# Optimization experiments

Measured on AMD Instinct MI355X. Metric: run time of the kernel, lower is better.

## Reference

```python
import jax, jax.numpy as jnp
import numpy as np

LAMBDA_SOFTMAX = 9.0
LAMBDA_LSE = 6.0
EPS = 1e-8
LEAKY_SLOPE = 0.1


def setup_inputs() -> dict:
    key = jax.random.key(0)
    k1, k2, k3, k4 = jax.random.split(key, 4)
    B, R, L, D = 256, 36, 40, 1024  # n_image=n_caption=B, n_regions, max_words, embed
    return {
        'pool_img': jax.random.normal(k1, (B, D), jnp.float32),
        'img_emb': jax.random.normal(k2, (B, R, D), jnp.float32),
        'pool_txt': jax.random.normal(k3, (B, D), jnp.float32),
        'cap_emb': jax.random.normal(k4, (B, L, D), jnp.float32),
    }


def _l2norm(x, axis):
    return x / (jnp.sqrt(jnp.sum(x * x, axis=axis, keepdims=True)) + EPS)


def _lse_reduce(m):
    # mul_(lambda_lse).exp_() ; sum over singleton dim ; log / lambda_lse
    return jnp.log(jnp.exp(m * LAMBDA_LSE)) / LAMBDA_LSE


def _text_score_one(cap_i, txt_poo_i, images):
    # cap_i: (L, d) query; images: (B, R, d) context. clipped_l2norm variant.
    attn = jnp.einsum('brd,ld->brl', images, cap_i)            # (B, R, L)
    attn = jax.nn.leaky_relu(attn, LEAKY_SLOPE)
    attn = _l2norm(attn, axis=2)                               # l2norm over queryL
    attn = jnp.swapaxes(attn, 1, 2)                            # (B, L, R)
    attn = jax.nn.softmax(attn * LAMBDA_SOFTMAX, axis=-1)      # softmax over regions
    wctx = jnp.einsum('blr,brd->bld', attn, images)            # (B, L, d)
    w12 = jnp.einsum('bld,d->bl', wctx, txt_poo_i)
    w1 = jnp.sqrt(jnp.sum(txt_poo_i * txt_poo_i))
    w2 = jnp.sqrt(jnp.sum(wctx * wctx, axis=2))
    sim = w12 / jnp.maximum(w1 * w2, EPS)                      # (B, L)
    return _lse_reduce(jnp.mean(sim, axis=1))                  # (B,)


def _image_score_one(cap_i, img_emb, img_poo):
    # query: img_emb (B, R, d); context: cap_i (L, d) broadcast over B.
    attn = jnp.einsum('ld,brd->blr', cap_i, img_emb)           # (B, L, R)
    attn = jax.nn.leaky_relu(attn, LEAKY_SLOPE)
    attn = _l2norm(attn, axis=2)                               # l2norm over regions
    attn = jnp.swapaxes(attn, 1, 2)                            # (B, R, L)
    attn = jax.nn.softmax(attn * LAMBDA_SOFTMAX, axis=-1)      # softmax over words
    wctx = jnp.einsum('brl,ld->brd', attn, cap_i)              # (B, R, d)
    w12 = jnp.einsum('brd,bd->br', wctx, img_poo)
    w1 = jnp.sqrt(jnp.sum(img_poo * img_poo, axis=1, keepdims=True))  # (B,1)
    w2 = jnp.sqrt(jnp.sum(wctx * wctx, axis=2))                # (B, R)
    sim = w12 / jnp.maximum(w1 * w2, EPS)
    return _lse_reduce(jnp.mean(sim, axis=1))                  # (B,)


def reference(pool_img, img_emb, pool_txt, cap_emb):
    # scores_t2i: loop over captions -> vmap; result (n_cap, n_image) -> transpose
    t2i = jax.vmap(_text_score_one, in_axes=(0, 0, None))(cap_emb, pool_txt, img_emb).T
    i2t = jax.vmap(_image_score_one, in_axes=(0, None, None))(cap_emb, img_emb, pool_img).T
    base = pool_img @ pool_txt.T
    return t2i + i2t + base
```

## Files before the change

kernel.cpp:

```cpp
#include <hip/hip_runtime.h>

typedef unsigned short u16;
typedef __attribute__((ext_vector_type(8))) short bf16x8;
typedef __attribute__((ext_vector_type(4))) float f32x4;

#define D_EMB 1024
#define NBAT  256
#define AS1 __attribute__((address_space(1)))
#define AS3 __attribute__((address_space(3)))

__device__ __forceinline__ u16 f2bf(float f){
    unsigned int u = __float_as_uint(f);
    unsigned int r = (u + 0x7fffu + ((u >> 16) & 1u)) >> 16;
    return (u16)r;
}
__device__ __forceinline__ float leaky(float x){ return x > 0.f ? x : 0.1f * x; }

__device__ __forceinline__ unsigned pack2(float a, float b){
    return (__float_as_uint(a) >> 16) | (__float_as_uint(b) & 0xffff0000u);
}

__global__ void pack_kernel(const float* __restrict__ pool_img, const float* __restrict__ img_emb,
                            const float* __restrict__ pool_txt, const float* __restrict__ cap_emb,
                            u16* __restrict__ imgw, u16* __restrict__ capw){
    int row = blockIdx.x;
    const float* src; u16* dst;
    if (row < NBAT * 37){
        int e = row / 37, rr = row - e * 37;
        src = (rr < 36) ? (img_emb + ((size_t)e * 36 + rr) * D_EMB) : (pool_img + (size_t)e * D_EMB);
        dst = imgw + (size_t)row * D_EMB;
    } else {
        int r2 = row - NBAT * 37;
        int e = r2 / 41, rr = r2 - e * 41;
        src = (rr < 40) ? (cap_emb + ((size_t)e * 40 + rr) * D_EMB) : (pool_txt + (size_t)e * D_EMB);
        dst = capw + (size_t)r2 * D_EMB;
    }
    int t = threadIdx.x;
    float4 v = ((const float4*)src)[t];
    unsigned long long pk = (unsigned long long)f2bf(v.x)
        | ((unsigned long long)f2bf(v.y) << 16)
        | ((unsigned long long)f2bf(v.z) << 32)
        | ((unsigned long long)f2bf(v.w) << 48);
    *(unsigned long long*)(dst + (size_t)t * 4) = pk;
}

__global__ void norm_kernel(const float* __restrict__ pool_img, const float* __restrict__ pool_txt,
                            float* __restrict__ w1i, float* __restrict__ w1t){
    __shared__ float red[256];
    int v = blockIdx.x;
    const float* src = (v < 256) ? (pool_img + (size_t)v * D_EMB)
                                 : (pool_txt + (size_t)(v - 256) * D_EMB);
    int t = threadIdx.x;
    float4 x = ((const float4*)src)[t];
    red[t] = x.x*x.x + x.y*x.y + x.z*x.z + x.w*x.w;
    __syncthreads();
    for (int off = 128; off > 0; off >>= 1){
        if (t < off) red[t] += red[t + off];
        __syncthreads();
    }
    if (t == 0){
        float n = sqrtf(red[0]);
        if (v < 256) w1i[v] = n; else w1t[v - 256] = n;
    }
}

__launch_bounds__(256, 2)
__global__ void gram_kernel(const u16* __restrict__ imgw, const u16* __restrict__ capw,
                            float* __restrict__ G, float* __restrict__ H){
    __shared__ __align__(16) char gsm[6144];
    int blk = blockIdx.x;
    int tid = threadIdx.x, lane = tid & 63;
    int wave = __builtin_amdgcn_readfirstlane(tid >> 6);
    int frow = lane & 15, q = lane >> 4;

    const u16* E; float* Gout; int R;
    if (blk < NBAT){ E = imgw + (size_t)blk * 37 * D_EMB; Gout = G + (size_t)blk * 1296; R = 36; }
    else { int b = blk - NBAT; E = capw + (size_t)b * 41 * D_EMB; Gout = H + (size_t)b * 1600; R = 40; }

    {
        uint4 z = {0u,0u,0u,0u};
        for (int off = tid * 16; off < 6144; off += 4096) *(uint4*)(gsm + off) = z;
    }

    const u16* gsrc[2]; int goff[2]; bool gval[2];
    #pragma unroll
    for (int j = 0; j < 2; ++j){
        int g = wave + j * 4;
        gval[j] = false; gsrc[j] = E; goff[j] = 0;
        if (g < 6){
            int kk = g / 3, t = g - kk * 3;
            int row = t * 16 + frow;
            gsrc[j] = E + (size_t)row * D_EMB + kk * 32 + q * 8;
            goff[j] = g * 1024;
            gval[j] = (row < R);
        }
    }

    int wm = wave >> 1, wn = wave & 1;
    int nTm = wm ? 1 : 2, nTn = wn ? 1 : 2;
    f32x4 acc[2][2];
    #pragma unroll
    for (int a = 0; a < 2; ++a)
        #pragma unroll
        for (int b = 0; b < 2; ++b) acc[a][b] = (f32x4){0.f,0.f,0.f,0.f};

    for (int c = 0; c < 16; ++c){
        __syncthreads();
        #pragma unroll
        for (int j = 0; j < 2; ++j){
            if (gval[j]){
                __builtin_amdgcn_global_load_lds(
                    (const AS1 void*)(const void*)(gsrc[j] + c * 64),
                    (AS3 void*)(void*)(gsm + goff[j] + lane * 16),
                    16, 0, 0);
            }
        }
        __syncthreads();
        #pragma unroll
        for (int kk = 0; kk < 2; ++kk){
            bf16x8 fA[2], fB[2];
            #pragma unroll
            for (int mi = 0; mi < 2; ++mi)
                if (mi < nTm) fA[mi] = *(const bf16x8*)(gsm + ((kk * 3 + (wm + mi * 2)) * 64 + lane) * 16);
            #pragma unroll
            for (int ni = 0; ni < 2; ++ni)
                if (ni < nTn) fB[ni] = *(const bf16x8*)(gsm + ((kk * 3 + (wn + ni * 2)) * 64 + lane) * 16);
            #pragma unroll
            for (int mi = 0; mi < 2; ++mi)
                if (mi < nTm)
                    #pragma unroll
                    for (int ni = 0; ni < 2; ++ni)
                        if (ni < nTn)
                            acc[mi][ni] = __builtin_amdgcn_mfma_f32_16x16x32_bf16(
                                fA[mi], fB[ni], acc[mi][ni], 0, 0, 0);
        }
    }

    #pragma unroll
    for (int mi = 0; mi < 2; ++mi){
        if (mi < nTm){
            int tm = wm + mi * 2;
            #pragma unroll
            for (int ni = 0; ni < 2; ++ni){
                if (ni < nTn){
                    int tn = wn + ni * 2;
                    int col = tn * 16 + frow;
                    if (col < R){
                        #pragma unroll
                        for (int g = 0; g < 4; ++g){
                            int row = tm * 16 + q * 4 + g;
                            if (row < R) Gout[row * R + col] = acc[mi][ni][g];
                        }
                    }
                }
            }
        }
    }
}

template<int R>
__device__ __forceinline__ void chol_wave(const float* __restrict__ src,
                                          u16* __restrict__ dst, int lane){
    int r = lane;
    bool act = (r < R);
    const float* row = src + (size_t)(act ? r : 0) * R;
    float a[R];
    #pragma unroll
    for (int k = 0; k < R; ++k) a[k] = act ? row[k] : 0.f;
    #pragma unroll
    for (int j = 0; j < R; ++j){
        float ajj = __shfl(a[j], j);
        float inv = (ajj > 1e-12f) ? rsqrtf(ajj) : 0.f;
        float lrj = a[j] * inv;
        if (r < j || !act) lrj = 0.f;
        dst[j * 64 + lane] = f2bf(lrj);
        #pragma unroll
        for (int k = j + 1; k < R; ++k){
            float lkj = __shfl(lrj, k);
            a[k] = fmaf(-lrj, lkj, a[k]);
        }
    }
    #pragma unroll
    for (int j = R; j < 48; ++j) dst[j * 64 + lane] = 0;
}

__global__ void chol_kernel(const float* __restrict__ G, const float* __restrict__ H,
                            u16* __restrict__ Lbi, u16* __restrict__ Lbc){
    int lane = threadIdx.x & 63;
    int wave = threadIdx.x >> 6;
    int id = blockIdx.x * 4 + wave;
    if (id < NBAT) chol_wave<36>(G + (size_t)id * 1296, Lbi + (size_t)id * 3072, lane);
    else           chol_wave<40>(H + (size_t)(id - NBAT) * 1600, Lbc + (size_t)(id - NBAT) * 3072, lane);
}

__launch_bounds__(256, 5)
__global__ void fused_kernel(const u16* __restrict__ imgw, const u16* __restrict__ capw,
                             const u16* __restrict__ Lbi, const u16* __restrict__ Lbc,
                             const float* __restrict__ w1i, const float* __restrict__ w1t,
                             float* __restrict__ out){
    __shared__ __align__(16) char smem[26624];
    float* Call = (float*)smem;
    float* rnb  = (float*)(smem + 25160);
    float* cnb  = (float*)(smem + 25736);

    int tid  = threadIdx.x;
    int lane = tid & 63;
    int wave = __builtin_amdgcn_readfirstlane(tid >> 6);
    int frow = lane & 15, q = lane >> 4;

    int lin = blockIdx.x;
    int xcd = lin & 7;
    int s   = lin >> 3;
    int b_t = (xcd << 4) | (s & 15);
    int i_t = s >> 4;
    int b0 = b_t * 2, i0 = i_t * 2;
    const u16* Ag = imgw + (size_t)b0 * 37 * D_EMB;
    const u16* Bg = capw + (size_t)i0 * 41 * D_EMB;

    {
        uint4 z = {0u,0u,0u,0u};
        for (int off = tid * 16; off < 22528; off += 4096) *(uint4*)(smem + off) = z;
    }

    const u16* gsrc[3]; int goff[3]; bool gval[3];
    #pragma unroll
    for (int j = 0; j < 3; ++j){
        int g = wave + j * 4;
        gval[j] = false; gsrc[j] = Ag; goff[j] = 0;
        if (g < 11){
            if (g < 5){
                int row = g * 16 + frow;
                gsrc[j] = Ag + (size_t)row * D_EMB + q * 8;
                goff[j] = g * 1024;
                gval[j] = (row < 74);
            } else {
                int gb = g - 5;
                int row = gb * 16 + frow;
                gsrc[j] = Bg + (size_t)row * D_EMB + q * 8;
                goff[j] = 5120 + gb * 1024;
                gval[j] = (row < 82);
            }
        }
    }

    int wm = wave >> 1, wn = wave & 1;
    int nTm = wm ? 2 : 3;
    f32x4 acc[3][3];
    #pragma unroll
    for (int aa = 0; aa < 3; ++aa)
        #pragma unroll
        for (int bb = 0; bb < 3; ++bb) acc[aa][bb] = (f32x4){0.f, 0.f, 0.f, 0.f};

    __syncthreads();

    #pragma unroll
    for (int j = 0; j < 3; ++j){
        if (gval[j]){
            __builtin_amdgcn_global_load_lds(
                (const AS1 void*)(const void*)(gsrc[j]),
                (AS3 void*)(void*)(smem + goff[j] + lane * 16),
                16, 0, 0);
        }
    }
    __syncthreads();

    for (int c = 0; c < 32; ++c){
        if (c < 31){
            int nb = ((c + 1) & 1) * 11264;
            #pragma unroll
            for (int j = 0; j < 3; ++j){
                if (gval[j]){
                    __builtin_amdgcn_global_load_lds(
                        (const AS1 void*)(const void*)(gsrc[j] + (c + 1) * 32),
                        (AS3 void*)(void*)(smem + nb + goff[j] + lane * 16),
                        16, 0, 0);
                }
            }
        }
        int cb = (c & 1) * 11264;
        bf16x8 bfr[3];
        #pragma unroll
        for (int ni = 0; ni < 3; ++ni){
            int tn = wn + ni * 2;
            bfr[ni] = *(const bf16x8*)(smem + cb + 5120 + tn * 1024 + lane * 16);
        }
        #pragma unroll
        for (int mi = 0; mi < 3; ++mi){
            if (mi < nTm){
                int tm = wm + mi * 2;
                bf16x8 af = *(const bf16x8*)(smem + cb + tm * 1024 + lane * 16);
                #pragma unroll
                for (int ni = 0; ni < 3; ++ni){
                    acc[mi][ni] = __builtin_amdgcn_mfma_f32_16x16x32_bf16(
                        af, bfr[ni], acc[mi][ni], 0, 0, 0);
                }
            }
        }
        __syncthreads();
    }

    #pragma unroll
    for (int mi = 0; mi < 3; ++mi){
        if (mi < nTm){
            int tm = wm + mi * 2;
            #pragma unroll
            for (int ni = 0; ni < 3; ++ni){
                int tn = wn + ni * 2;
                int col = tn * 16 + frow;
                int rbase = tm * 16 + q * 4;
                if (col < 82){
                    #pragma unroll
                    for (int g = 0; g < 4; ++g){
                        int rowc = rbase + g;
                        if (rowc < 74) Call[rowc * 85 + col] = acc[mi][ni][g];
                    }
                }
            }
        }
    }
    __syncthreads();

    int pb = wave >> 1, pi = wave & 1;
    int bg = b0 + pb, ig = i0 + pi;
    const float* Sv = Call + (pb * 37) * 85 + pi * 41;
    const u16* Lb_t2i = Lbi + (size_t)bg * 3072;
    const u16* Lb_i2t = Lbc + (size_t)ig * 3072;

    {
        int r0 = (lane < 36) ? lane : 35;
        float s2 = 0.f;
        #pragma unroll
        for (int l = 0; l < 40; ++l){ float x = leaky(Sv[r0 * 85 + l]); s2 = fmaf(x, x, s2); }
        if (lane < 36) rnb[wave * 36 + lane] = 1.f / (sqrtf(s2) + 1e-8f);
    }
    {
        int l0 = (lane < 40) ? lane : 39;
        float s2 = 0.f;
        #pragma unroll
        for (int r = 0; r < 36; ++r){ float x = leaky(Sv[r * 85 + l0]); s2 = fmaf(x, x, s2); }
        if (lane < 40) cnb[wave * 40 + lane] = 1.f / (sqrtf(s2) + 1e-8f);
    }

    unsigned up[18]; float num1 = 0.f;
    {
        int lc = (lane < 40) ? lane : 39;
        #pragma unroll
        for (int r = 0; r < 36; r += 2){
            float x0 = leaky(Sv[r * 85 + lc]) * rnb[wave * 36 + r];
            float x1 = leaky(Sv[(r + 1) * 85 + lc]) * rnb[wave * 36 + r + 1];
            float e0 = __expf(9.0f * x0), e1 = __expf(9.0f * x1);
            num1 = fmaf(e0, Sv[r * 85 + 40], fmaf(e1, Sv[(r + 1) * 85 + 40], num1));
            up[r >> 1] = pack2(e0, e1);
        }
    }
    unsigned vp[20]; float num2 = 0.f;
    {
        int rc = (lane < 36) ? lane : 35;
        #pragma unroll
        for (int l = 0; l < 40; l += 2){
            float x0 = leaky(Sv[rc * 85 + l]) * cnb[wave * 40 + l];
            float x1 = leaky(Sv[rc * 85 + l + 1]) * cnb[wave * 40 + l + 1];
            float e0 = __expf(9.0f * x0), e1 = __expf(9.0f * x1);
            num2 = fmaf(e0, Sv[36 * 85 + l], fmaf(e1, Sv[36 * 85 + l + 1], num2));
            vp[l >> 1] = pack2(e0, e1);
        }
    }
    float base = Sv[36 * 85 + 40];
    __syncthreads();

    char* slice = smem + wave * 6144;
    int sxw = lane & 7;

    if (lane < 40){
        char* rp = slice + lane * 128;
        #pragma unroll
        for (int jj = 0; jj < 9; ++jj){
            int slot = jj >> 1, wi = (jj & 1) * 8;
            uint2 w; w.x = up[jj * 2]; w.y = up[jj * 2 + 1];
            *(uint2*)(rp + ((slot ^ sxw) * 16 + wi)) = w;
        }
        uint2 z2; z2.x = 0u; z2.y = 0u;
        *(uint2*)(rp + ((4 ^ sxw) * 16 + 8)) = z2;
        uint4 z4 = {0u,0u,0u,0u};
        #pragma unroll
        for (int slot = 5; slot < 8; ++slot)
            *(uint4*)(rp + ((slot ^ sxw) * 16)) = z4;
    }

    float tsum;
    {
        f32x4 pacc[3][3];
        #pragma unroll
        for (int aa = 0; aa < 3; ++aa)
            #pragma unroll
            for (int bb = 0; bb < 3; ++bb) pacc[aa][bb] = (f32x4){0.f,0.f,0.f,0.f};
        #pragma unroll
        for (int kk = 0; kk < 2; ++kk){
            bf16x8 afr[3];
            #pragma unroll
            for (int mt = 0; mt < 3; ++mt){
                int row = mt * 16 + frow;
                afr[mt] = *(const bf16x8*)(slice + row * 128 + (((kk * 4 + q) ^ (row & 7)) * 16));
            }
            #pragma unroll
            for (int nt = 0; nt < 3; ++nt){
                bf16x8 bfr = *(const bf16x8*)(Lb_t2i + (nt * 16 + frow) * 64 + kk * 32 + q * 8);
                #pragma unroll
                for (int mt = 0; mt < 3; ++mt)
                    pacc[mt][nt] = __builtin_amdgcn_mfma_f32_16x16x32_bf16(
                        afr[mt], bfr, pacc[mt][nt], 0, 0, 0);
            }
        }
        float w1 = w1t[ig];
        tsum = 0.f;
        #pragma unroll
        for (int mt = 0; mt < 3; ++mt){
            #pragma unroll
            for (int g = 0; g < 4; ++g){
                float sv = pacc[mt][0][g] * pacc[mt][0][g]
                         + pacc[mt][1][g] * pacc[mt][1][g];
                float t2 = pacc[mt][2][g] * pacc[mt][2][g];
                sv += (frow < 4) ? t2 : 0.f;
                sv += __shfl_xor(sv, 1); sv += __shfl_xor(sv, 2);
                sv += __shfl_xor(sv, 4); sv += __shfl_xor(sv, 8);
                int m = mt * 16 + 4 * q + g;
                float nm = __shfl(num1, m);
                float sim = nm / fmaxf(w1 * sqrtf(sv), 1e-8f);
                tsum += (m < 40) ? sim : 0.f;
            }
        }
        tsum += __shfl_xor(tsum, 16);
        tsum += __shfl_xor(tsum, 32);
    }

    if (lane < 36){
        char* rp = slice + lane * 128;
        #pragma unroll
        for (int jj = 0; jj < 10; ++jj){
            int slot = jj >> 1, wi = (jj & 1) * 8;
            uint2 w; w.x = vp[jj * 2]; w.y = vp[jj * 2 + 1];
            *(uint2*)(rp + ((slot ^ sxw) * 16 + wi)) = w;
        }
        uint4 z4 = {0u,0u,0u,0u};
        #pragma unroll
        for (int slot = 5; slot < 8; ++slot)
            *(uint4*)(rp + ((slot ^ sxw) * 16)) = z4;
    }

    float isum;
    {
        f32x4 pacc[3][3];
        #pragma unroll
        for (int aa = 0; aa < 3; ++aa)
            #pragma unroll
            for (int bb = 0; bb < 3; ++bb) pacc[aa][bb] = (f32x4){0.f,0.f,0.f,0.f};
        #pragma unroll
        for (int kk = 0; kk < 2; ++kk){
            bf16x8 afr[3];
            #pragma unroll
            for (int mt = 0; mt < 3; ++mt){
                int row = mt * 16 + frow;
                afr[mt] = *(const bf16x8*)(slice + row * 128 + (((kk * 4 + q) ^ (row & 7)) * 16));
            }
            #pragma unroll
            for (int nt = 0; nt < 3; ++nt){
                bf16x8 bfr = *(const bf16x8*)(Lb_i2t + (nt * 16 + frow) * 64 + kk * 32 + q * 8);
                #pragma unroll
                for (int mt = 0; mt < 3; ++mt)
                    pacc[mt][nt] = __builtin_amdgcn_mfma_f32_16x16x32_bf16(
                        afr[mt], bfr, pacc[mt][nt], 0, 0, 0);
            }
        }
        float w1 = w1i[bg];
        isum = 0.f;
        #pragma unroll
        for (int mt = 0; mt < 3; ++mt){
            #pragma unroll
            for (int g = 0; g < 4; ++g){
                float sv = pacc[mt][0][g] * pacc[mt][0][g]
                         + pacc[mt][1][g] * pacc[mt][1][g];
                float t2 = pacc[mt][2][g] * pacc[mt][2][g];
                sv += (frow < 8) ? t2 : 0.f;
                sv += __shfl_xor(sv, 1); sv += __shfl_xor(sv, 2);
                sv += __shfl_xor(sv, 4); sv += __shfl_xor(sv, 8);
                int m = mt * 16 + 4 * q + g;
                float nm = __shfl(num2, m);
                float sim = nm / fmaxf(w1 * sqrtf(sv), 1e-8f);
                isum += (m < 36) ? sim : 0.f;
            }
        }
        isum += __shfl_xor(isum, 16);
        isum += __shfl_xor(isum, 32);
    }

    if (lane == 0)
        out[bg * 256 + ig] = tsum * (1.f / 40.f) + isum * (1.f / 36.f) + base;
}

extern "C" void kernel_launch(void* const* d_in, const int* in_sizes, int n_in,
                              void* d_out, int out_size, void* d_ws, size_t ws_size,
                              hipStream_t stream){
    const float* pool_img = (const float*)d_in[0];
    const float* img_emb  = (const float*)d_in[1];
    const float* pool_txt = (const float*)d_in[2];
    const float* cap_emb  = (const float*)d_in[3];
    float* out = (float*)d_out;

    char* ws = (char*)d_ws;
    size_t o = 0;
    u16* imgw = (u16*)(ws + o);  o += (size_t)256 * 37 * 1024 * 2;
    u16* capw = (u16*)(ws + o);  o += (size_t)256 * 41 * 1024 * 2;
    float* G  = (float*)(ws + o); o += (size_t)256 * 36 * 36 * 4;
    float* H  = (float*)(ws + o); o += (size_t)256 * 40 * 40 * 4;
    float* w1i = (float*)(ws + o); o += 1024;
    float* w1t = (float*)(ws + o); o += 1024;
    u16* Lbi = (u16*)(ws + o); o += (size_t)256 * 48 * 64 * 2;
    u16* Lbc = (u16*)(ws + o); o += (size_t)256 * 48 * 64 * 2;

    pack_kernel<<<19968, 256, 0, stream>>>(pool_img, img_emb, pool_txt, cap_emb, imgw, capw);
    norm_kernel<<<512, 256, 0, stream>>>(pool_img, pool_txt, w1i, w1t);
    gram_kernel<<<512, 256, 0, stream>>>(imgw, capw, G, H);
    chol_kernel<<<128, 256, 0, stream>>>(G, H, Lbi, Lbc);
    fused_kernel<<<16384, 256, 0, stream>>>(imgw, capw, Lbi, Lbc, w1i, w1t, out);
}
```

Baseline: 872.6 us.

## Build MFMA A-fragments in registers and fold numerator into spare MFMA column

Exponentiated attention weights are now computed directly in the MFMA A-fragment layout in registers, replacing the earlier pass that wrote packed bf16 rows to a swizzled LDS slice and read them back. The per-row numerator (weights dotted with the pooled-vector projection) is no longer accumulated in fp32 on the side. It is obtained by placing the projection values in an unused B column of the last MFMA tile. This drops LDS stores and loads plus a barrier, but recomputes the exp and leaky_relu work for each fragment and computes the numerator in bf16 rather than fp32, which may change accuracy.

```diff
diff --git a/kernel.cpp b/kernel.cpp
--- a/kernel.cpp
+++ b/kernel.cpp
@@ -3,6 +3,7 @@
 typedef unsigned short u16;
 typedef __attribute__((ext_vector_type(8))) short bf16x8;
 typedef __attribute__((ext_vector_type(4))) float f32x4;
+typedef __attribute__((ext_vector_type(4))) unsigned u32x4;
 
 #define D_EMB 1024
 #define NBAT  256
@@ -340,52 +341,7 @@
         for (int r = 0; r < 36; ++r){ float x = leaky(Sv[r * 85 + l0]); s2 = fmaf(x, x, s2); }
         if (lane < 40) cnb[wave * 40 + lane] = 1.f / (sqrtf(s2) + 1e-8f);
     }
-
-    unsigned up[18]; float num1 = 0.f;
-    {
-        int lc = (lane < 40) ? lane : 39;
-        #pragma unroll
-        for (int r = 0; r < 36; r += 2){
-            float x0 = leaky(Sv[r * 85 + lc]) * rnb[wave * 36 + r];
-            float x1 = leaky(Sv[(r + 1) * 85 + lc]) * rnb[wave * 36 + r + 1];
-            float e0 = __expf(9.0f * x0), e1 = __expf(9.0f * x1);
-            num1 = fmaf(e0, Sv[r * 85 + 40], fmaf(e1, Sv[(r + 1) * 85 + 40], num1));
-            up[r >> 1] = pack2(e0, e1);
-        }
-    }
-    unsigned vp[20]; float num2 = 0.f;
-    {
-        int rc = (lane < 36) ? lane : 35;
-        #pragma unroll
-        for (int l = 0; l < 40; l += 2){
-            float x0 = leaky(Sv[rc * 85 + l]) * cnb[wave * 40 + l];
-            float x1 = leaky(Sv[rc * 85 + l + 1]) * cnb[wave * 40 + l + 1];
-            float e0 = __expf(9.0f * x0), e1 = __expf(9.0f * x1);
-            num2 = fmaf(e0, Sv[36 * 85 + l], fmaf(e1, Sv[36 * 85 + l + 1], num2));
-            vp[l >> 1] = pack2(e0, e1);
-        }
-    }
     float base = Sv[36 * 85 + 40];
-    __syncthreads();
-
-    char* slice = smem + wave * 6144;
-    int sxw = lane & 7;
-
-    if (lane < 40){
-        char* rp = slice + lane * 128;
-        #pragma unroll
-        for (int jj = 0; jj < 9; ++jj){
-            int slot = jj >> 1, wi = (jj & 1) * 8;
-            uint2 w; w.x = up[jj * 2]; w.y = up[jj * 2 + 1];
-            *(uint2*)(rp + ((slot ^ sxw) * 16 + wi)) = w;
-        }
-        uint2 z2; z2.x = 0u; z2.y = 0u;
-        *(uint2*)(rp + ((4 ^ sxw) * 16 + 8)) = z2;
-        uint4 z4 = {0u,0u,0u,0u};
-        #pragma unroll
-        for (int slot = 5; slot < 8; ++slot)
-            *(uint4*)(rp + ((slot ^ sxw) * 16)) = z4;
-    }
 
     float tsum;
     {
@@ -396,15 +352,43 @@
             for (int bb = 0; bb < 3; ++bb) pacc[aa][bb] = (f32x4){0.f,0.f,0.f,0.f};
         #pragma unroll
         for (int kk = 0; kk < 2; ++kk){
+            float rn[8];
+            #pragma unroll
+            for (int j = 0; j < 8; ++j){
+                int k = kk * 32 + q * 8 + j;
+                int kc = (k < 36) ? k : 35;
+                rn[j] = (k < 36) ? rnb[wave * 36 + kc] : 0.f;
+            }
+            u32x4 pw;
+            #pragma unroll
+            for (int jj = 0; jj < 4; ++jj){
+                int k0 = kk * 32 + q * 8 + jj * 2, k1 = k0 + 1;
+                int c0 = (k0 < 36) ? k0 : 35, c1 = (k1 < 36) ? k1 : 35;
+                float p0 = (k0 < 36) ? Sv[c0 * 85 + 40] : 0.f;
+                float p1 = (k1 < 36) ? Sv[c1 * 85 + 40] : 0.f;
+                pw[jj] = pack2(p0, p1);
+            }
             bf16x8 afr[3];
             #pragma unroll
             for (int mt = 0; mt < 3; ++mt){
-                int row = mt * 16 + frow;
-                afr[mt] = *(const bf16x8*)(slice + row * 128 + (((kk * 4 + q) ^ (row & 7)) * 16));
+                int m = mt * 16 + frow;
+                u32x4 aw;
+                #pragma unroll
+                for (int jj = 0; jj < 4; ++jj){
+                    int k0 = kk * 32 + q * 8 + jj * 2, k1 = k0 + 1;
+                    int c0 = (k0 < 36) ? k0 : 35, c1 = (k1 < 36) ? k1 : 35;
+                    float e0 = __expf(9.f * leaky(Sv[c0 * 85 + m]) * rn[jj * 2]);
+                    float e1 = __expf(9.f * leaky(Sv[c1 * 85 + m]) * rn[jj * 2 + 1]);
+                    e0 = (k0 < 36) ? e0 : 0.f;
+                    e1 = (k1 < 36) ? e1 : 0.f;
+                    aw[jj] = pack2(e0, e1);
+                }
+                afr[mt] = __builtin_bit_cast(bf16x8, aw);
             }
             #pragma unroll
             for (int nt = 0; nt < 3; ++nt){
                 bf16x8 bfr = *(const bf16x8*)(Lb_t2i + (nt * 16 + frow) * 64 + kk * 32 + q * 8);
+                if (nt == 2 && frow == 4) bfr = __builtin_bit_cast(bf16x8, pw);
                 #pragma unroll
                 for (int mt = 0; mt < 3; ++mt)
                     pacc[mt][nt] = __builtin_amdgcn_mfma_f32_16x16x32_bf16(
@@ -423,28 +407,14 @@
                 sv += (frow < 4) ? t2 : 0.f;
                 sv += __shfl_xor(sv, 1); sv += __shfl_xor(sv, 2);
                 sv += __shfl_xor(sv, 4); sv += __shfl_xor(sv, 8);
+                float nm = __shfl(pacc[mt][2][g], (lane & 48) + 4);
                 int m = mt * 16 + 4 * q + g;
-                float nm = __shfl(num1, m);
                 float sim = nm / fmaxf(w1 * sqrtf(sv), 1e-8f);
                 tsum += (m < 40) ? sim : 0.f;
             }
         }
         tsum += __shfl_xor(tsum, 16);
         tsum += __shfl_xor(tsum, 32);
-    }
-
-    if (lane < 36){
-        char* rp = slice + lane * 128;
-        #pragma unroll
-        for (int jj = 0; jj < 10; ++jj){
-            int slot = jj >> 1, wi = (jj & 1) * 8;
-            uint2 w; w.x = vp[jj * 2]; w.y = vp[jj * 2 + 1];
-            *(uint2*)(rp + ((slot ^ sxw) * 16 + wi)) = w;
-        }
-        uint4 z4 = {0u,0u,0u,0u};
-        #pragma unroll
-        for (int slot = 5; slot < 8; ++slot)
-            *(uint4*)(rp + ((slot ^ sxw) * 16)) = z4;
     }
 
     float isum;
@@ -456,15 +426,44 @@
             for (int bb = 0; bb < 3; ++bb) pacc[aa][bb] = (f32x4){0.f,0.f,0.f,0.f};
         #pragma unroll
         for (int kk = 0; kk < 2; ++kk){
+            float cn[8];
+            #pragma unroll
+            for (int j = 0; j < 8; ++j){
+                int k = kk * 32 + q * 8 + j;
+                int kc = (k < 40) ? k : 39;
+                cn[j] = (k < 40) ? cnb[wave * 40 + kc] : 0.f;
+            }
+            u32x4 qw;
+            #pragma unroll
+            for (int jj = 0; jj < 4; ++jj){
+                int k0 = kk * 32 + q * 8 + jj * 2, k1 = k0 + 1;
+                int c0 = (k0 < 40) ? k0 : 39, c1 = (k1 < 40) ? k1 : 39;
+                float q0 = (k0 < 40) ? Sv[36 * 85 + c0] : 0.f;
+                float q1 = (k1 < 40) ? Sv[36 * 85 + c1] : 0.f;
+                qw[jj] = pack2(q0, q1);
+            }
             bf16x8 afr[3];
             #pragma unroll
             for (int mt = 0; mt < 3; ++mt){
-                int row = mt * 16 + frow;
-                afr[mt] = *(const bf16x8*)(slice + row * 128 + (((kk * 4 + q) ^ (row & 7)) * 16));
+                int m = mt * 16 + frow;
+                int mr = (m < 36) ? m : 35;
+                u32x4 aw;
+                #pragma unroll
+                for (int jj = 0; jj < 4; ++jj){
+                    int k0 = kk * 32 + q * 8 + jj * 2, k1 = k0 + 1;
+                    int c0 = (k0 < 40) ? k0 : 39, c1 = (k1 < 40) ? k1 : 39;
+                    float e0 = __expf(9.f * leaky(Sv[mr * 85 + c0]) * cn[jj * 2]);
+                    float e1 = __expf(9.f * leaky(Sv[mr * 85 + c1]) * cn[jj * 2 + 1]);
+                    e0 = (k0 < 40) ? e0 : 0.f;
+                    e1 = (k1 < 40) ? e1 : 0.f;
+                    aw[jj] = pack2(e0, e1);
+                }
+                afr[mt] = __builtin_bit_cast(bf16x8, aw);
             }
             #pragma unroll
             for (int nt = 0; nt < 3; ++nt){
                 bf16x8 bfr = *(const bf16x8*)(Lb_i2t + (nt * 16 + frow) * 64 + kk * 32 + q * 8);
+                if (nt == 2 && frow == 8) bfr = __builtin_bit_cast(bf16x8, qw);
                 #pragma unroll
                 for (int mt = 0; mt < 3; ++mt)
                     pacc[mt][nt] = __builtin_amdgcn_mfma_f32_16x16x32_bf16(
@@ -483,8 +482,8 @@
                 sv += (frow < 8) ? t2 : 0.f;
                 sv += __shfl_xor(sv, 1); sv += __shfl_xor(sv, 2);
                 sv += __shfl_xor(sv, 4); sv += __shfl_xor(sv, 8);
+                float nm = __shfl(pacc[mt][2][g], (lane & 48) + 8);
                 int m = mt * 16 + 4 * q + g;
-                float nm = __shfl(num2, m);
                 float sim = nm / fmaxf(w1 * sqrtf(sv), 1e-8f);
                 isum += (m < 36) ? sim : 0.f;
             }
```

Result: faster. 809.5 us (-7.2%).
